# Optimization experiments

Hardware: AMD Instinct MI355X
Metric: run time of the kernel (lower is better)

Reference implementation:

```python
import jax, jax.numpy as jnp
import numpy as np
from functools import partial

N_NODES = 50000


def gcn_conv(x, row, col, norm, W, b, num_nodes):
    # x: [N, Fin], W: [Fout, Fin] (torch Linear weight layout), b: [Fout]
    h = x @ W.T                                   # [N, Fout]
    msg = norm[:, None] * h[row]                  # per-edge message, gather x_j = x[row]
    out = jax.ops.segment_sum(msg, col, num_segments=num_nodes)  # scatter-add to target col
    return out + b


def _build_norm(row, col, edge_weight, num_nodes):
    # add self-loops with weight 1.0
    loops = jnp.arange(num_nodes, dtype=row.dtype)
    row_f = jnp.concatenate([row, loops])
    col_f = jnp.concatenate([col, loops])
    ew_f = jnp.concatenate([edge_weight, jnp.ones((num_nodes,), edge_weight.dtype)])
    # degree counts occurrences of row (unweighted, like PyG degree())
    deg = jax.ops.segment_sum(jnp.ones_like(ew_f), row_f, num_segments=num_nodes)
    dinv = jnp.where(deg > 0, deg ** -0.5, 0.0).astype(edge_weight.dtype)
    norm = dinv[row_f] * ew_f * dinv[col_f]
    return row_f, col_f, norm


def setup_inputs() -> dict:
    key = jax.random.key(0)
    k = jax.random.split(key, 8)
    N, E = N_NODES, 800000
    Fin, H, C = 256, 96, 40
    x = jax.random.normal(k[0], (N, Fin), dtype=jnp.float32)
    edge_index = jax.random.randint(k[1], (2, E), 0, N, dtype=jnp.int64)
    edge_weight = jax.random.uniform(k[2], (E,), dtype=jnp.float32)
    W1 = jax.random.normal(k[3], (H, Fin), dtype=jnp.float32) * (1.0 / np.sqrt(Fin))
    b1 = jnp.zeros((H,), jnp.float32)
    W2 = jax.random.normal(k[4], (C, H), dtype=jnp.float32) * (1.0 / np.sqrt(H))
    b2 = jnp.zeros((C,), jnp.float32)
    return {"x": x, "edge_index": edge_index, "edge_weight": edge_weight,
            "W1": W1, "b1": b1, "W2": W2, "b2": b2}


def reference(x, edge_index, edge_weight, W1, b1, W2, b2):
    N = x.shape[0]
    row, col = edge_index[0], edge_index[1]
    row_f, col_f, norm = _build_norm(row, col, edge_weight, N)
    h = jax.nn.relu(gcn_conv(x, row_f, col_f, norm, W1, b1, N))
    # dropout is identity in eval mode
    out = gcn_conv(h, row_f, col_f, norm, W2, b2, N)
    return jax.nn.log_softmax(out, axis=1)
```

## Files before the change

kernel.cpp:

```cpp
#include <hip/hip_runtime.h>
#include <hip/hip_bf16.h>
#include <hip/hip_fp16.h>
#include <math.h>

#define NN 50000
#define EE 800000
#define FIN 256
#define FH 96
#define FC 40
#define NBK 196

typedef _Float16 h4 __attribute__((ext_vector_type(4)));
typedef _Float16 h8 __attribute__((ext_vector_type(8)));
typedef float f32x4 __attribute__((ext_vector_type(4)));

__device__ __forceinline__ unsigned pack_edge(int row, float w) {
    _Float16 he = (_Float16)w;
    unsigned short us;
    __builtin_memcpy(&us, &he, 2);
    return (unsigned)row | ((unsigned)us << 16);
}
__device__ __forceinline__ float unpack_w(unsigned pk) {
    unsigned short us = (unsigned short)(pk >> 16);
    _Float16 hv;
    __builtin_memcpy(&hv, &us, 2);
    return (float)hv;
}


#define G1B 782

__global__ __launch_bounds__(256) void k_fused1(const float* __restrict__ x,
                                                const float* __restrict__ W,
                                                _Float16* __restrict__ g0h,
                                                const int* __restrict__ ei, int E,
                                                unsigned* __restrict__ copies,
                                                unsigned* __restrict__ bcnt2d, int n) {
    __shared__ unsigned lds[6250];
    int bid = blockIdx.x;
    int tid = threadIdx.x;

    if (bid < G1B) {
        _Float16* xsp = (_Float16*)lds;
        _Float16* wsp = xsp + 64 * 72;
        int row0 = bid * 64;
        int l = tid & 63, w = tid >> 6;
        int l15 = l & 15, lg = l >> 4;

        f32x4 acc[6];
#pragma unroll
        for (int c = 0; c < 6; ++c) acc[c] = (f32x4)0.f;

        float4 px[4], pw[6];
        {
#pragma unroll
            for (int i = 0; i < 4; ++i) {
                int it = tid + 256 * i;
                int r = it >> 4, k4 = it & 15;
                int gr = row0 + r;
                px[i] = make_float4(0.f, 0.f, 0.f, 0.f);
                if (gr < n) px[i] = *(const float4*)&x[gr * FIN + k4 * 4];
            }
#pragma unroll
            for (int i = 0; i < 6; ++i) {
                int it = tid + 256 * i;
                int r = it >> 4, k4 = it & 15;
                pw[i] = *(const float4*)&W[r * FIN + k4 * 4];
            }
        }
        for (int kc = 0; kc < 4; ++kc) {
#pragma unroll
            for (int i = 0; i < 4; ++i) {
                int it = tid + 256 * i;
                int r = it >> 4, k4 = it & 15;
                h4 hv = {(_Float16)px[i].x, (_Float16)px[i].y, (_Float16)px[i].z, (_Float16)px[i].w};
                *(h4*)&xsp[r * 72 + k4 * 4] = hv;
            }
#pragma unroll
            for (int i = 0; i < 6; ++i) {
                int it = tid + 256 * i;
                int r = it >> 4, k4 = it & 15;
                h4 hv = {(_Float16)pw[i].x, (_Float16)pw[i].y, (_Float16)pw[i].z, (_Float16)pw[i].w};
                *(h4*)&wsp[r * 72 + k4 * 4] = hv;
            }
            if (kc < 3) {
                int kbase = (kc + 1) * 64;
#pragma unroll
                for (int i = 0; i < 4; ++i) {
                    int it = tid + 256 * i;
                    int r = it >> 4, k4 = it & 15;
                    int gr = row0 + r;
                    px[i] = make_float4(0.f, 0.f, 0.f, 0.f);
                    if (gr < n) px[i] = *(const float4*)&x[gr * FIN + kbase + k4 * 4];
                }
#pragma unroll
                for (int i = 0; i < 6; ++i) {
                    int it = tid + 256 * i;
                    int r = it >> 4, k4 = it & 15;
                    pw[i] = *(const float4*)&W[r * FIN + kbase + k4 * 4];
                }
            }
            __syncthreads();
#pragma unroll
            for (int ks = 0; ks < 2; ++ks) {
                h8 a = *(const h8*)&xsp[(16 * w + l15) * 72 + ks * 32 + lg * 8];
#pragma unroll
                for (int ct = 0; ct < 6; ++ct) {
                    h8 b = *(const h8*)&wsp[(ct * 16 + l15) * 72 + ks * 32 + lg * 8];
                    acc[ct] = __builtin_amdgcn_mfma_f32_16x16x32_f16(a, b, acc[ct], 0, 0, 0);
                }
            }
            __syncthreads();
        }
#pragma unroll
        for (int r = 0; r < 4; ++r) {
            int grow = row0 + 16 * w + lg * 4 + r;
            if (grow < n) {
#pragma unroll
                for (int ct = 0; ct < 6; ++ct)
                    g0h[(size_t)grow * FH + ct * 16 + l15] = (_Float16)acc[ct][r];
            }
        }
    } else if (bid < 910) {
        int b2 = bid - G1B;
        int half = b2 >> 6;
        int slice = b2 & 63;
        int ES = (E + 63) >> 6;
        const int* ptr = ei;
        for (int i = tid; i < 6250; i += 256) lds[i] = 0u;
        __syncthreads();
        int lo = slice * ES, hi = min(lo + ES, E);
        int nlo = half * 25000;
        for (int i = lo + tid; i < hi; i += 256) {
            int rel = ptr[i] - nlo;
            if ((unsigned)rel < 25000u)
                atomicAdd(&lds[rel >> 2], 1u << ((rel & 3) << 3));
        }
        __syncthreads();
        unsigned* dst = copies + (size_t)b2 * 6250;
        for (int i = tid; i < 6250; i += 256) dst[i] = lds[i];
    } else {
        int chunk = bid - 910;
        int ES = (E + 63) >> 6;
        const int* col = ei + E;
        for (int i = tid; i < NBK; i += 256) lds[i] = 0u;
        __syncthreads();
        int lo = chunk * ES, hi = min(lo + ES, E);
        for (int i = lo + tid; i < hi; i += 256) atomicAdd(&lds[col[i] >> 8], 1u);
        __syncthreads();
        for (int i = tid; i < NBK; i += 256) bcnt2d[chunk * 256 + i] = lds[i];
    }
}


__global__ __launch_bounds__(256) void k_reduce(const unsigned* __restrict__ copies,
                                                const unsigned* __restrict__ bcnt2d,
                                                float* __restrict__ dinv,
                                                unsigned* __restrict__ bstart,
                                                unsigned* __restrict__ gcur,
                                                unsigned* __restrict__ off, unsigned E) {
    int t = blockIdx.x * blockDim.x + threadIdx.x;
    if (t < 12500) {
        int half = t / 6250, w = t - half * 6250;
        unsigned s0 = 0, s1 = 0, s2 = 0, s3 = 0;
        const unsigned* br = copies + (size_t)(half * 64) * 6250 + w;
#pragma unroll 8
        for (int s = 0; s < 64; ++s) {
            unsigned v = br[s * 6250];
            s0 += v & 0xffu;
            s1 += (v >> 8) & 0xffu;
            s2 += (v >> 16) & 0xffu;
            s3 += (v >> 24);
        }
        int n0 = half * 25000 + 4 * w;
        dinv[n0 + 0] = rsqrtf((float)(s0 + 1u));
        dinv[n0 + 1] = rsqrtf((float)(s1 + 1u));
        dinv[n0 + 2] = rsqrtf((float)(s2 + 1u));
        dinv[n0 + 3] = rsqrtf((float)(s3 + 1u));
    }
    if (blockIdx.x == 0) {
        __shared__ unsigned sb[256];
        int tt = threadIdx.x;
        unsigned v = 0;
        if (tt < NBK) {
#pragma unroll 8
            for (int c = 0; c < 64; ++c) v += bcnt2d[c * 256 + tt];
        }
        sb[tt] = v;
        __syncthreads();
        for (int o = 1; o < 256; o <<= 1) {
            unsigned tv = (tt >= o) ? sb[tt - o] : 0u;
            __syncthreads();
            sb[tt] += tv;
            __syncthreads();
        }
        if (tt < NBK) {
            unsigned ex = sb[tt] - v;
            bstart[tt] = ex;
            gcur[tt] = ex;
            bstart[tt + 1] = sb[tt];
        }
        if (tt == 0) off[NN] = E;
    }
}


__global__ __launch_bounds__(256) void k_bucket(const int* __restrict__ row,
                                                const int* __restrict__ col,
                                                const float* __restrict__ ew,
                                                const float* __restrict__ dinv,
                                                unsigned* __restrict__ gcur,
                                                unsigned* __restrict__ bkc,
                                                unsigned* __restrict__ bkpk, int E) {
    __shared__ unsigned cnt[NBK];
    __shared__ unsigned cur[NBK];
    int tid = threadIdx.x;
    int CH = (E + gridDim.x - 1) / gridDim.x;
    int lo = blockIdx.x * CH, hi = min(lo + CH, E);
    for (int i = tid; i < NBK; i += 256) cnt[i] = 0u;
    __syncthreads();
    for (int i = lo + tid; i < hi; i += 256) atomicAdd(&cnt[col[i] >> 8], 1u);
    __syncthreads();
    for (int i = tid; i < NBK; i += 256) cur[i] = atomicAdd(&gcur[i], cnt[i]);
    __syncthreads();
    for (int i = lo + tid; i < hi; i += 256) {
        int c = col[i];
        int r = row[i];
        unsigned pos = atomicAdd(&cur[c >> 8], 1u);
        bkc[pos] = (unsigned)c;
        bkpk[pos] = pack_edge(r, dinv[r] * ew[i]);
    }
}


__global__ __launch_bounds__(256) void k_place(const unsigned* __restrict__ bkc,
                                               const unsigned* __restrict__ bkpk,
                                               const unsigned* __restrict__ bstart,
                                               unsigned* __restrict__ off,
                                               unsigned* __restrict__ epk, int n) {
    __shared__ unsigned cnt[256];
    __shared__ unsigned cur[256];
    int b = blockIdx.x;
    int tid = threadIdx.x;
    int node0 = b * 256;
    unsigned st = bstart[b], en = bstart[b + 1];
    cnt[tid] = 0u;
    __syncthreads();
    for (unsigned i = st + tid; i < en; i += 256) atomicAdd(&cnt[bkc[i] & 255], 1u);
    __syncthreads();
    unsigned v = cnt[tid];
    cur[tid] = v;
    __syncthreads();
    for (int o = 1; o < 256; o <<= 1) {
        unsigned tv = (tid >= o) ? cur[tid - o] : 0u;
        __syncthreads();
        cur[tid] += tv;
        __syncthreads();
    }
    unsigned base = st + cur[tid] - v;
    int node = node0 + tid;
    if (node < n) off[node] = base;
    cur[tid] = base;
    __syncthreads();
    for (unsigned i = st + tid; i < en; i += 256) {
        unsigned c = bkc[i];
        unsigned pos = atomicAdd(&cur[c & 255], 1u);
        epk[pos] = bkpk[i];
    }
}


__global__ __launch_bounds__(256) void k_agg96(const _Float16* __restrict__ g0h,
                                               const unsigned* __restrict__ off,
                                               const unsigned* __restrict__ epk,
                                               const float* __restrict__ dinv,
                                               const float* __restrict__ b,
                                               _Float16* __restrict__ outh, int n) {
    int tid = blockIdx.x * 256 + threadIdx.x;
    int node = tid / 12;
    int f8 = tid - node * 12;
    if (node >= n) return;
    float s = dinv[node];
    const h8* gp = (const h8*)g0h;
    h8 self = gp[(size_t)node * 12 + f8];
    float acc[8];
#pragma unroll
    for (int j = 0; j < 8; ++j) acc[j] = s * (float)self[j];
    unsigned st = off[node], en = off[node + 1];
    unsigned e = st;
    for (; e + 8 <= en; e += 8) {
        unsigned k0 = epk[e + 0], k1 = epk[e + 1], k2 = epk[e + 2], k3 = epk[e + 3];
        unsigned k4 = epk[e + 4], k5 = epk[e + 5], k6 = epk[e + 6], k7 = epk[e + 7];
        h8 ga = gp[(size_t)(k0 & 0xffffu) * 12 + f8];
        h8 gb = gp[(size_t)(k1 & 0xffffu) * 12 + f8];
        h8 gc = gp[(size_t)(k2 & 0xffffu) * 12 + f8];
        h8 gd = gp[(size_t)(k3 & 0xffffu) * 12 + f8];
        h8 ge = gp[(size_t)(k4 & 0xffffu) * 12 + f8];
        h8 gf = gp[(size_t)(k5 & 0xffffu) * 12 + f8];
        h8 gg = gp[(size_t)(k6 & 0xffffu) * 12 + f8];
        h8 gh = gp[(size_t)(k7 & 0xffffu) * 12 + f8];
        float w0 = unpack_w(k0), w1 = unpack_w(k1), w2 = unpack_w(k2), w3 = unpack_w(k3);
        float w4 = unpack_w(k4), w5 = unpack_w(k5), w6 = unpack_w(k6), w7 = unpack_w(k7);
#pragma unroll
        for (int j = 0; j < 8; ++j) acc[j] = fmaf(w0, (float)ga[j], acc[j]);
#pragma unroll
        for (int j = 0; j < 8; ++j) acc[j] = fmaf(w1, (float)gb[j], acc[j]);
#pragma unroll
        for (int j = 0; j < 8; ++j) acc[j] = fmaf(w2, (float)gc[j], acc[j]);
#pragma unroll
        for (int j = 0; j < 8; ++j) acc[j] = fmaf(w3, (float)gd[j], acc[j]);
#pragma unroll
        for (int j = 0; j < 8; ++j) acc[j] = fmaf(w4, (float)ge[j], acc[j]);
#pragma unroll
        for (int j = 0; j < 8; ++j) acc[j] = fmaf(w5, (float)gf[j], acc[j]);
#pragma unroll
        for (int j = 0; j < 8; ++j) acc[j] = fmaf(w6, (float)gg[j], acc[j]);
#pragma unroll
        for (int j = 0; j < 8; ++j) acc[j] = fmaf(w7, (float)gh[j], acc[j]);
    }
    for (; e + 4 <= en; e += 4) {
        unsigned k0 = epk[e + 0], k1 = epk[e + 1], k2 = epk[e + 2], k3 = epk[e + 3];
        h8 ga = gp[(size_t)(k0 & 0xffffu) * 12 + f8];
        h8 gb = gp[(size_t)(k1 & 0xffffu) * 12 + f8];
        h8 gc = gp[(size_t)(k2 & 0xffffu) * 12 + f8];
        h8 gd = gp[(size_t)(k3 & 0xffffu) * 12 + f8];
        float w0 = unpack_w(k0), w1 = unpack_w(k1), w2 = unpack_w(k2), w3 = unpack_w(k3);
#pragma unroll
        for (int j = 0; j < 8; ++j) acc[j] = fmaf(w0, (float)ga[j], acc[j]);
#pragma unroll
        for (int j = 0; j < 8; ++j) acc[j] = fmaf(w1, (float)gb[j], acc[j]);
#pragma unroll
        for (int j = 0; j < 8; ++j) acc[j] = fmaf(w2, (float)gc[j], acc[j]);
#pragma unroll
        for (int j = 0; j < 8; ++j) acc[j] = fmaf(w3, (float)gd[j], acc[j]);
    }
    for (; e < en; ++e) {
        unsigned k = epk[e];
        h8 g = gp[(size_t)(k & 0xffffu) * 12 + f8];
        float wv = unpack_w(k);
#pragma unroll
        for (int j = 0; j < 8; ++j) acc[j] = fmaf(wv, (float)g[j], acc[j]);
    }
    float4 bv0 = ((const float4*)b)[f8 * 2];
    float4 bv1 = ((const float4*)b)[f8 * 2 + 1];
    const float bb[8] = {bv0.x, bv0.y, bv0.z, bv0.w, bv1.x, bv1.y, bv1.z, bv1.w};
    h8 o;
#pragma unroll
    for (int j = 0; j < 8; ++j) o[j] = (_Float16)fmaxf(fmaf(s, acc[j], bb[j]), 0.f);
    *(h8*)&outh[(size_t)node * FH + f8 * 8] = o;
}


__global__ __launch_bounds__(256) void k_gemm2(const _Float16* __restrict__ h,
                                               const float* __restrict__ W2,
                                               _Float16* __restrict__ g1h, int n) {
    __shared__ _Float16 hs[64][104];
    __shared__ _Float16 wsm[48][104];
    int tid = threadIdx.x;
    int row0 = blockIdx.x * 64;
    int l = tid & 63, w = tid >> 6;
    int l15 = l & 15, lg = l >> 4;

    f32x4 acc[3];
#pragma unroll
    for (int c = 0; c < 3; ++c) acc[c] = (f32x4)0.f;

#pragma unroll
    for (int i = 0; i < 6; ++i) {
        int it = tid + 256 * i;
        int r = it / 24, k4 = it - r * 24;
        int gr = row0 + r;
        h4 hv = {(_Float16)0.f, (_Float16)0.f, (_Float16)0.f, (_Float16)0.f};
        if (gr < n) hv = *(const h4*)&h[(size_t)gr * FH + k4 * 4];
        *(h4*)&hs[r][k4 * 4] = hv;
    }
#pragma unroll
    for (int i = 0; i < 5; ++i) {
        int it = tid + 256 * i;
        if (it < 1152) {
            int r = it / 24, k4 = it - r * 24;
            h4 hv = {(_Float16)0.f, (_Float16)0.f, (_Float16)0.f, (_Float16)0.f};
            if (r < FC) {
                float4 v = *(const float4*)&W2[r * FH + k4 * 4];
                hv[0] = (_Float16)v.x; hv[1] = (_Float16)v.y;
                hv[2] = (_Float16)v.z; hv[3] = (_Float16)v.w;
            }
            *(h4*)&wsm[r][k4 * 4] = hv;
        }
    }
    __syncthreads();
#pragma unroll
    for (int ks = 0; ks < 3; ++ks) {
        h8 a = *(const h8*)&hs[16 * w + l15][ks * 32 + lg * 8];
#pragma unroll
        for (int ct = 0; ct < 3; ++ct) {
            h8 b = *(const h8*)&wsm[ct * 16 + l15][ks * 32 + lg * 8];
            acc[ct] = __builtin_amdgcn_mfma_f32_16x16x32_f16(a, b, acc[ct], 0, 0, 0);
        }
    }
#pragma unroll
    for (int r = 0; r < 4; ++r) {
        int grow = row0 + 16 * w + lg * 4 + r;
        if (grow < n) {
#pragma unroll
            for (int ct = 0; ct < 3; ++ct) {
                int colc = ct * 16 + l15;
                if (colc < FC)
                    g1h[(size_t)grow * FC + colc] = (_Float16)acc[ct][r];
            }
        }
    }
}


__global__ __launch_bounds__(256) void k_agg40lsm(const _Float16* __restrict__ g1h,
                                                  const unsigned* __restrict__ off,
                                                  const unsigned* __restrict__ epk,
                                                  const float* __restrict__ dinv,
                                                  const float* __restrict__ b,
                                                  float* __restrict__ out, int n) {
    __shared__ float sm[50][41];
    int tid = threadIdx.x;
    int ln = tid / 5;
    int f8 = tid - ln * 5;
    int node = blockIdx.x * 50 + ln;
    bool active = (tid < 250) && (node < n);
    float acc[8];
#pragma unroll
    for (int j = 0; j < 8; ++j) acc[j] = 0.f;
    if (active) {
        float s = dinv[node];
        const h8* gp = (const h8*)g1h;
        h8 self = gp[(size_t)node * 5 + f8];
#pragma unroll
        for (int j = 0; j < 8; ++j) acc[j] = s * (float)self[j];
        unsigned st = off[node], en = off[node + 1];
        unsigned e = st;
        for (; e + 4 <= en; e += 4) {
            unsigned k0 = epk[e + 0], k1 = epk[e + 1], k2 = epk[e + 2], k3 = epk[e + 3];
            h8 ga = gp[(size_t)(k0 & 0xffffu) * 5 + f8];
            h8 gb = gp[(size_t)(k1 & 0xffffu) * 5 + f8];
            h8 gc = gp[(size_t)(k2 & 0xffffu) * 5 + f8];
            h8 gd = gp[(size_t)(k3 & 0xffffu) * 5 + f8];
            float w0 = unpack_w(k0), w1 = unpack_w(k1), w2 = unpack_w(k2), w3 = unpack_w(k3);
#pragma unroll
            for (int j = 0; j < 8; ++j) acc[j] = fmaf(w0, (float)ga[j], acc[j]);
#pragma unroll
            for (int j = 0; j < 8; ++j) acc[j] = fmaf(w1, (float)gb[j], acc[j]);
#pragma unroll
            for (int j = 0; j < 8; ++j) acc[j] = fmaf(w2, (float)gc[j], acc[j]);
#pragma unroll
            for (int j = 0; j < 8; ++j) acc[j] = fmaf(w3, (float)gd[j], acc[j]);
        }
        for (; e < en; ++e) {
            unsigned k = epk[e];
            h8 g = gp[(size_t)(k & 0xffffu) * 5 + f8];
            float wv = unpack_w(k);
#pragma unroll
            for (int j = 0; j < 8; ++j) acc[j] = fmaf(wv, (float)g[j], acc[j]);
        }
        float4 bv0 = ((const float4*)b)[f8 * 2];
        float4 bv1 = ((const float4*)b)[f8 * 2 + 1];
        const float bb[8] = {bv0.x, bv0.y, bv0.z, bv0.w, bv1.x, bv1.y, bv1.z, bv1.w};
#pragma unroll
        for (int j = 0; j < 8; ++j) {
            acc[j] = fmaf(s, acc[j], bb[j]);
            sm[ln][f8 * 8 + j] = acc[j];
        }
    }
    __syncthreads();
    if (tid < 50) {
        int nd = blockIdx.x * 50 + tid;
        if (nd < n) {
            float m = -INFINITY;
#pragma unroll 8
            for (int j = 0; j < FC; ++j) m = fmaxf(m, sm[tid][j]);
            float sum = 0.f;
#pragma unroll 8
            for (int j = 0; j < FC; ++j) sum += expf(sm[tid][j] - m);
            sm[tid][40] = logf(sum) + m;
        }
    }
    __syncthreads();
    if (active) {
        float lse = sm[ln][40];
        float4 o0 = make_float4(acc[0] - lse, acc[1] - lse, acc[2] - lse, acc[3] - lse);
        float4 o1 = make_float4(acc[4] - lse, acc[5] - lse, acc[6] - lse, acc[7] - lse);
        *(float4*)&out[(size_t)node * FC + f8 * 8] = o0;
        *(float4*)&out[(size_t)node * FC + f8 * 8 + 4] = o1;
    }
}


extern "C" void kernel_launch(void* const* d_in, const int* in_sizes, int n_in,
                              void* d_out, int out_size, void* d_ws, size_t ws_size,
                              hipStream_t stream) {
    const float* x  = (const float*)d_in[0];
    const int*   ei = (const int*)d_in[1];
    const float* ew = (const float*)d_in[2];
    const float* W1 = (const float*)d_in[3];
    const float* b1 = (const float*)d_in[4];
    const float* W2 = (const float*)d_in[5];
    const float* b2 = (const float*)d_in[6];
    float* out = (float*)d_out;

    const int N = NN;
    const int E = in_sizes[1] / 2;
    const int* row = ei;
    const int* col = ei + E;

    float* ws = (float*)d_ws;
    float*    dinv   = (float*)(ws + 0);
    unsigned* off    = (unsigned*)(ws + 50176);
    unsigned* bcnt2d = (unsigned*)(ws + 100480);
    unsigned* bstart = (unsigned*)(ws + 116864);
    unsigned* gcur   = (unsigned*)(ws + 117120);
    unsigned* copies = (unsigned*)(ws + 150976);
    unsigned* bkc    = (unsigned*)(ws + 150976);
    unsigned* bkpk   = (unsigned*)(ws + 950976);
    _Float16* h      = (_Float16*)(ws + 150976);
    unsigned* epk    = (unsigned*)(ws + 4950976);
    _Float16* g0h    = (_Float16*)(ws + 6550976);
    _Float16* g1h    = (_Float16*)(ws + 8950976);

    const int B = 256;

    hipLaunchKernelGGL(k_fused1, dim3(974), dim3(B), 0, stream,
                       x, W1, g0h, ei, E, copies, bcnt2d, N);
    hipLaunchKernelGGL(k_reduce, dim3(49), dim3(B), 0, stream,
                       copies, bcnt2d, dinv, bstart, gcur, off, (unsigned)E);

    hipLaunchKernelGGL(k_bucket, dim3(320), dim3(B), 0, stream,
                       row, col, ew, dinv, gcur, bkc, bkpk, E);
    hipLaunchKernelGGL(k_place, dim3(NBK), dim3(B), 0, stream, bkc, bkpk, bstart, off, epk, N);

    hipLaunchKernelGGL(k_agg96, dim3((N * 12 + B - 1) / B), dim3(B), 0, stream,
                       g0h, off, epk, dinv, b1, h, N);

    hipLaunchKernelGGL(k_gemm2, dim3((N + 63) / 64), dim3(B), 0, stream, h, W2, g1h, N);

    hipLaunchKernelGGL(k_agg40lsm, dim3((N + 49) / 50), dim3(B), 0, stream,
                       g1h, off, epk, dinv, b2, out, N);
}
```

Before: 124.0 us.

## Move GEMM1 from histogram kernel into bucket kernel to rebalance stages

The first-layer GEMM blocks move out of the fused histogram/count kernel and are co-launched with the edge-bucketing blocks in one kernel. The histogram kernel becomes a small 192-block launch, so the reduce step that depends on it can start sooner, and the GEMM work overlaps with the bucket scatter instead. LDS use per block grows in the combined kernel because the xsp/wsp arrays and the cnt/cur arrays are now separate statics, which may lower occupancy. The bucket blocks are now scheduled after the 782 GEMM blocks, which could delay the bucket path.

```diff
diff --git a/kernel.cpp b/kernel.cpp
--- a/kernel.cpp
+++ b/kernel.cpp
@@ -28,104 +28,16 @@
 }
 
 
-#define G1B 782
-
-__global__ __launch_bounds__(256) void k_fused1(const float* __restrict__ x,
-                                                const float* __restrict__ W,
-                                                _Float16* __restrict__ g0h,
-                                                const int* __restrict__ ei, int E,
-                                                unsigned* __restrict__ copies,
-                                                unsigned* __restrict__ bcnt2d, int n) {
+__global__ __launch_bounds__(256) void k_histcnt(const int* __restrict__ ei, int E,
+                                                 unsigned* __restrict__ copies,
+                                                 unsigned* __restrict__ bcnt2d) {
     __shared__ unsigned lds[6250];
     int bid = blockIdx.x;
     int tid = threadIdx.x;
-
-    if (bid < G1B) {
-        _Float16* xsp = (_Float16*)lds;
-        _Float16* wsp = xsp + 64 * 72;
-        int row0 = bid * 64;
-        int l = tid & 63, w = tid >> 6;
-        int l15 = l & 15, lg = l >> 4;
-
-        f32x4 acc[6];
-#pragma unroll
-        for (int c = 0; c < 6; ++c) acc[c] = (f32x4)0.f;
-
-        float4 px[4], pw[6];
-        {
-#pragma unroll
-            for (int i = 0; i < 4; ++i) {
-                int it = tid + 256 * i;
-                int r = it >> 4, k4 = it & 15;
-                int gr = row0 + r;
-                px[i] = make_float4(0.f, 0.f, 0.f, 0.f);
-                if (gr < n) px[i] = *(const float4*)&x[gr * FIN + k4 * 4];
-            }
-#pragma unroll
-            for (int i = 0; i < 6; ++i) {
-                int it = tid + 256 * i;
-                int r = it >> 4, k4 = it & 15;
-                pw[i] = *(const float4*)&W[r * FIN + k4 * 4];
-            }
-        }
-        for (int kc = 0; kc < 4; ++kc) {
-#pragma unroll
-            for (int i = 0; i < 4; ++i) {
-                int it = tid + 256 * i;
-                int r = it >> 4, k4 = it & 15;
-                h4 hv = {(_Float16)px[i].x, (_Float16)px[i].y, (_Float16)px[i].z, (_Float16)px[i].w};
-                *(h4*)&xsp[r * 72 + k4 * 4] = hv;
-            }
-#pragma unroll
-            for (int i = 0; i < 6; ++i) {
-                int it = tid + 256 * i;
-                int r = it >> 4, k4 = it & 15;
-                h4 hv = {(_Float16)pw[i].x, (_Float16)pw[i].y, (_Float16)pw[i].z, (_Float16)pw[i].w};
-                *(h4*)&wsp[r * 72 + k4 * 4] = hv;
-            }
-            if (kc < 3) {
-                int kbase = (kc + 1) * 64;
-#pragma unroll
-                for (int i = 0; i < 4; ++i) {
-                    int it = tid + 256 * i;
-                    int r = it >> 4, k4 = it & 15;
-                    int gr = row0 + r;
-                    px[i] = make_float4(0.f, 0.f, 0.f, 0.f);
-                    if (gr < n) px[i] = *(const float4*)&x[gr * FIN + kbase + k4 * 4];
-                }
-#pragma unroll
-                for (int i = 0; i < 6; ++i) {
-                    int it = tid + 256 * i;
-                    int r = it >> 4, k4 = it & 15;
-                    pw[i] = *(const float4*)&W[r * FIN + kbase + k4 * 4];
-                }
-            }
-            __syncthreads();
-#pragma unroll
-            for (int ks = 0; ks < 2; ++ks) {
-                h8 a = *(const h8*)&xsp[(16 * w + l15) * 72 + ks * 32 + lg * 8];
-#pragma unroll
-                for (int ct = 0; ct < 6; ++ct) {
-                    h8 b = *(const h8*)&wsp[(ct * 16 + l15) * 72 + ks * 32 + lg * 8];
-                    acc[ct] = __builtin_amdgcn_mfma_f32_16x16x32_f16(a, b, acc[ct], 0, 0, 0);
-                }
-            }
-            __syncthreads();
-        }
-#pragma unroll
-        for (int r = 0; r < 4; ++r) {
-            int grow = row0 + 16 * w + lg * 4 + r;
-            if (grow < n) {
-#pragma unroll
-                for (int ct = 0; ct < 6; ++ct)
-                    g0h[(size_t)grow * FH + ct * 16 + l15] = (_Float16)acc[ct][r];
-            }
-        }
-    } else if (bid < 910) {
-        int b2 = bid - G1B;
-        int half = b2 >> 6;
-        int slice = b2 & 63;
-        int ES = (E + 63) >> 6;
+    int ES = (E + 63) >> 6;
+    if (bid < 128) {
+        int half = bid >> 6;
+        int slice = bid & 63;
         const int* ptr = ei;
         for (int i = tid; i < 6250; i += 256) lds[i] = 0u;
         __syncthreads();
@@ -137,11 +49,10 @@
                 atomicAdd(&lds[rel >> 2], 1u << ((rel & 3) << 3));
         }
         __syncthreads();
-        unsigned* dst = copies + (size_t)b2 * 6250;
+        unsigned* dst = copies + (size_t)bid * 6250;
         for (int i = tid; i < 6250; i += 256) dst[i] = lds[i];
     } else {
-        int chunk = bid - 910;
-        int ES = (E + 63) >> 6;
+        int chunk = bid - 128;
         const int* col = ei + E;
         for (int i = tid; i < NBK; i += 256) lds[i] = 0u;
         __syncthreads();
@@ -205,30 +116,121 @@
 }
 
 
-__global__ __launch_bounds__(256) void k_bucket(const int* __restrict__ row,
-                                                const int* __restrict__ col,
-                                                const float* __restrict__ ew,
-                                                const float* __restrict__ dinv,
-                                                unsigned* __restrict__ gcur,
-                                                unsigned* __restrict__ bkc,
-                                                unsigned* __restrict__ bkpk, int E) {
+#define G1B 782
+
+__global__ __launch_bounds__(256) void k_gemm1bkt(const float* __restrict__ x,
+                                                  const float* __restrict__ W,
+                                                  _Float16* __restrict__ g0h,
+                                                  const int* __restrict__ ei,
+                                                  const float* __restrict__ ew,
+                                                  const float* __restrict__ dinv,
+                                                  unsigned* __restrict__ gcur,
+                                                  unsigned* __restrict__ bkc,
+                                                  unsigned* __restrict__ bkpk,
+                                                  int E, int n) {
+    __shared__ _Float16 xsp[64 * 72];
+    __shared__ _Float16 wsp[96 * 72];
     __shared__ unsigned cnt[NBK];
     __shared__ unsigned cur[NBK];
+    int bid = blockIdx.x;
     int tid = threadIdx.x;
-    int CH = (E + gridDim.x - 1) / gridDim.x;
-    int lo = blockIdx.x * CH, hi = min(lo + CH, E);
-    for (int i = tid; i < NBK; i += 256) cnt[i] = 0u;
-    __syncthreads();
-    for (int i = lo + tid; i < hi; i += 256) atomicAdd(&cnt[col[i] >> 8], 1u);
-    __syncthreads();
-    for (int i = tid; i < NBK; i += 256) cur[i] = atomicAdd(&gcur[i], cnt[i]);
-    __syncthreads();
-    for (int i = lo + tid; i < hi; i += 256) {
-        int c = col[i];
-        int r = row[i];
-        unsigned pos = atomicAdd(&cur[c >> 8], 1u);
-        bkc[pos] = (unsigned)c;
-        bkpk[pos] = pack_edge(r, dinv[r] * ew[i]);
+
+    if (bid < G1B) {
+        int row0 = bid * 64;
+        int l = tid & 63, w = tid >> 6;
+        int l15 = l & 15, lg = l >> 4;
+
+        f32x4 acc[6];
+#pragma unroll
+        for (int c = 0; c < 6; ++c) acc[c] = (f32x4)0.f;
+
+        float4 px[4], pw[6];
+#pragma unroll
+        for (int i = 0; i < 4; ++i) {
+            int it = tid + 256 * i;
+            int r = it >> 4, k4 = it & 15;
+            int gr = row0 + r;
+            px[i] = make_float4(0.f, 0.f, 0.f, 0.f);
+            if (gr < n) px[i] = *(const float4*)&x[gr * FIN + k4 * 4];
+        }
+#pragma unroll
+        for (int i = 0; i < 6; ++i) {
+            int it = tid + 256 * i;
+            int r = it >> 4, k4 = it & 15;
+            pw[i] = *(const float4*)&W[r * FIN + k4 * 4];
+        }
+        for (int kc = 0; kc < 4; ++kc) {
+#pragma unroll
+            for (int i = 0; i < 4; ++i) {
+                int it = tid + 256 * i;
+                int r = it >> 4, k4 = it & 15;
+                h4 hv = {(_Float16)px[i].x, (_Float16)px[i].y, (_Float16)px[i].z, (_Float16)px[i].w};
+                *(h4*)&xsp[r * 72 + k4 * 4] = hv;
+            }
+#pragma unroll
+            for (int i = 0; i < 6; ++i) {
+                int it = tid + 256 * i;
+                int r = it >> 4, k4 = it & 15;
+                h4 hv = {(_Float16)pw[i].x, (_Float16)pw[i].y, (_Float16)pw[i].z, (_Float16)pw[i].w};
+                *(h4*)&wsp[r * 72 + k4 * 4] = hv;
+            }
+            if (kc < 3) {
+                int kbase = (kc + 1) * 64;
+#pragma unroll
+                for (int i = 0; i < 4; ++i) {
+                    int it = tid + 256 * i;
+                    int r = it >> 4, k4 = it & 15;
+                    int gr = row0 + r;
+                    px[i] = make_float4(0.f, 0.f, 0.f, 0.f);
+                    if (gr < n) px[i] = *(const float4*)&x[gr * FIN + kbase + k4 * 4];
+                }
+#pragma unroll
+                for (int i = 0; i < 6; ++i) {
+                    int it = tid + 256 * i;
+                    int r = it >> 4, k4 = it & 15;
+                    pw[i] = *(const float4*)&W[r * FIN + kbase + k4 * 4];
+                }
+            }
+            __syncthreads();
+#pragma unroll
+            for (int ks = 0; ks < 2; ++ks) {
+                h8 a = *(const h8*)&xsp[(16 * w + l15) * 72 + ks * 32 + lg * 8];
+#pragma unroll
+                for (int ct = 0; ct < 6; ++ct) {
+                    h8 b = *(const h8*)&wsp[(ct * 16 + l15) * 72 + ks * 32 + lg * 8];
+                    acc[ct] = __builtin_amdgcn_mfma_f32_16x16x32_f16(a, b, acc[ct], 0, 0, 0);
+                }
+            }
+            __syncthreads();
+        }
+#pragma unroll
+        for (int r = 0; r < 4; ++r) {
+            int grow = row0 + 16 * w + lg * 4 + r;
+            if (grow < n) {
+#pragma unroll
+                for (int ct = 0; ct < 6; ++ct)
+                    g0h[(size_t)grow * FH + ct * 16 + l15] = (_Float16)acc[ct][r];
+            }
+        }
+    } else {
+        const int* row = ei;
+        const int* col = ei + E;
+        int CH = (E + 319) / 320;
+        int chunk = bid - G1B;
+        int lo = chunk * CH, hi = min(lo + CH, E);
+        for (int i = tid; i < NBK; i += 256) cnt[i] = 0u;
+        __syncthreads();
+        for (int i = lo + tid; i < hi; i += 256) atomicAdd(&cnt[col[i] >> 8], 1u);
+        __syncthreads();
+        for (int i = tid; i < NBK; i += 256) cur[i] = atomicAdd(&gcur[i], cnt[i]);
+        __syncthreads();
+        for (int i = lo + tid; i < hi; i += 256) {
+            int c = col[i];
+            int r = row[i];
+            unsigned pos = atomicAdd(&cur[c >> 8], 1u);
+            bkc[pos] = (unsigned)c;
+            bkpk[pos] = pack_edge(r, dinv[r] * ew[i]);
+        }
     }
 }
 
@@ -506,8 +508,6 @@
 
     const int N = NN;
     const int E = in_sizes[1] / 2;
-    const int* row = ei;
-    const int* col = ei + E;
 
     float* ws = (float*)d_ws;
     float*    dinv   = (float*)(ws + 0);
@@ -525,13 +525,13 @@
 
     const int B = 256;
 
-    hipLaunchKernelGGL(k_fused1, dim3(974), dim3(B), 0, stream,
-                       x, W1, g0h, ei, E, copies, bcnt2d, N);
+    hipLaunchKernelGGL(k_histcnt, dim3(192), dim3(B), 0, stream, ei, E, copies, bcnt2d);
     hipLaunchKernelGGL(k_reduce, dim3(49), dim3(B), 0, stream,
                        copies, bcnt2d, dinv, bstart, gcur, off, (unsigned)E);
 
-    hipLaunchKernelGGL(k_bucket, dim3(320), dim3(B), 0, stream,
-                       row, col, ew, dinv, gcur, bkc, bkpk, E);
+    hipLaunchKernelGGL(k_gemm1bkt, dim3(G1B + 320), dim3(B), 0, stream,
+                       x, W1, g0h, ei, ew, dinv, gcur, bkc, bkpk, E, N);
+
     hipLaunchKernelGGL(k_place, dim3(NBK), dim3(B), 0, stream, bkc, bkpk, bstart, off, epk, N);
 
     hipLaunchKernelGGL(k_agg96, dim3((N * 12 + B - 1) / B), dim3(B), 0, stream,
```

Measured after the change: 130.7 us. +5.4%, slower.
